# Kernel tuning notes

Hardware: AMD Instinct MI355X
Metric: run time of the kernel (lower is better)

## Reference

```python
import jax, jax.numpy as jnp
import numpy as np

B, T, D = 1, 2048, 1024
H = 16
HD = D // H
K = 4
FF = 4 * D
LAYERS = 24
EPS = 1.1920929e-07  # torch.finfo(float32).eps, RMSNorm default


def setup_inputs() -> dict:
    key = jax.random.key(0)
    ks = jax.random.split(key, 16)
    s = 0.02
    return {
        "x": jax.random.normal(ks[0], (B, T, D), jnp.float32),
        "gamma": jax.random.uniform(ks[1], (D,), jnp.float32),
        "beta": jax.random.normal(ks[2], (D,), jnp.float32) * 0.1,
        "iter_scale": jax.random.uniform(ks[3], (1,), jnp.float32),
        "qkv_bases": jax.random.normal(ks[4], (K, 3 * D, D), jnp.float32) * s,
        "o_bases": jax.random.normal(ks[5], (K, D, D), jnp.float32) * s,
        "gate_bases": jax.random.normal(ks[6], (K, FF, D), jnp.float32) * s,
        "up_bases": jax.random.normal(ks[7], (K, FF, D), jnp.float32) * s,
        "down_bases": jax.random.normal(ks[8], (K, D, FF), jnp.float32) * s,
        "alpha_qkv": jax.random.normal(ks[9], (LAYERS, K), jnp.float32) * 0.1 + jnp.eye(LAYERS, K)[:, :K] * 0.0 + jnp.concatenate([jnp.ones((LAYERS, 1)), jnp.zeros((LAYERS, K - 1))], axis=1),
        "alpha_o": jnp.concatenate([jnp.ones((LAYERS, 1)), jnp.zeros((LAYERS, K - 1))], axis=1) + jax.random.normal(ks[10], (LAYERS, K)) * 0.1,
        "alpha_gate": jnp.concatenate([jnp.ones((LAYERS, 1)), jnp.zeros((LAYERS, K - 1))], axis=1) + jax.random.normal(ks[11], (LAYERS, K)) * 0.1,
        "alpha_up": jnp.concatenate([jnp.ones((LAYERS, 1)), jnp.zeros((LAYERS, K - 1))], axis=1) + jax.random.normal(ks[12], (LAYERS, K)) * 0.1,
        "alpha_down": jnp.concatenate([jnp.ones((LAYERS, 1)), jnp.zeros((LAYERS, K - 1))], axis=1) + jax.random.normal(ks[13], (LAYERS, K)) * 0.1,
        "norm1_w": jnp.ones((D,), jnp.float32),
        "norm2_w": jnp.ones((D,), jnp.float32),
        "layer_idx": 5,
    }


def _rmsnorm(x, w):
    return x * jax.lax.rsqrt(jnp.mean(x * x, axis=-1, keepdims=True) + EPS) * w


def reference(x, gamma, beta, iter_scale, qkv_bases, o_bases, gate_bases, up_bases,
              down_bases, alpha_qkv, alpha_o, alpha_gate, alpha_up, alpha_down,
              norm1_w, norm2_w, layer_idx):
    Bx, Tx, Dx = x.shape
    # --- attention sub-block ---
    h = _rmsnorm(x, norm1_w) * gamma + beta
    W_qkv = jnp.einsum('k,kij->ij', alpha_qkv[layer_idx], qkv_bases)  # [3D, D]
    qkv = jnp.einsum('btd,od->bto', h, W_qkv).reshape(Bx, Tx, 3, H, HD)
    qkv = jnp.transpose(qkv, (2, 0, 3, 1, 4))  # [3, B, H, T, HD]
    q, k, v = qkv[0], qkv[1], qkv[2]
    scores = jnp.einsum('bhqd,bhkd->bhqk', q, k) / jnp.sqrt(jnp.asarray(HD, x.dtype))
    causal = jnp.tril(jnp.ones((Tx, Tx), bool))
    scores = jnp.where(causal, scores, jnp.asarray(-jnp.inf, scores.dtype))
    attn = jax.nn.softmax(scores, axis=-1)
    out = jnp.einsum('bhqk,bhkd->bhqd', attn, v)
    out = jnp.transpose(out, (0, 2, 1, 3)).reshape(Bx, Tx, Dx)
    W_o = jnp.einsum('k,kij->ij', alpha_o[layer_idx], o_bases)
    x_attn = x + jnp.einsum('btd,od->bto', out, W_o)
    # --- SwiGLU FFN sub-block ---
    h2 = _rmsnorm(x_attn, norm2_w) * gamma + beta
    W_g = jnp.einsum('k,kij->ij', alpha_gate[layer_idx], gate_bases)
    W_u = jnp.einsum('k,kij->ij', alpha_up[layer_idx], up_bases)
    W_d = jnp.einsum('k,kij->ij', alpha_down[layer_idx], down_bases)
    gate = jnp.einsum('btd,fd->btf', h2, W_g)
    up = jnp.einsum('btd,fd->btf', h2, W_u)
    ffn_out = jnp.einsum('btf,df->btd', jax.nn.silu(gate) * up, W_d)
    block_out = x_attn + ffn_out
    return x + (block_out - x) * iter_scale
```

## Files before the change

### kernel.cpp

```cpp
#include <hip/hip_runtime.h>
#include <hip/hip_bf16.h>
#include <math.h>

typedef __bf16 bf16;
typedef __bf16 bf16x8 __attribute__((ext_vector_type(8)));
typedef __bf16 bf16x4 __attribute__((ext_vector_type(4)));
typedef float f32x4 __attribute__((ext_vector_type(4)));

#define EPSc 1.1920929e-07f
#define LOG2E 1.44269504f

static __device__ __forceinline__ void glds16(const void* g, void* l) {
  __builtin_amdgcn_global_load_lds((const __attribute__((address_space(1))) void*)g,
                                   (__attribute__((address_space(3))) void*)l, 16, 0, 0);
}

static __device__ __forceinline__ bf16x4 comb4(const float* b0, const float* b1,
                                               const float* b2, const float* b3,
                                               float a0, float a1, float a2, float a3) {
  float4 v0 = *(const float4*)b0, v1 = *(const float4*)b1;
  float4 v2 = *(const float4*)b2, v3 = *(const float4*)b3;
  bf16x4 o;
  o[0] = (bf16)(a0*v0.x + a1*v1.x + a2*v2.x + a3*v3.x);
  o[1] = (bf16)(a0*v0.y + a1*v1.y + a2*v2.y + a3*v3.y);
  o[2] = (bf16)(a0*v0.z + a1*v1.z + a2*v2.z + a3*v3.z);
  o[3] = (bf16)(a0*v0.w + a1*v1.w + a2*v2.w + a3*v3.w);
  return o;
}

__global__ __launch_bounds__(256)
void prep1(const float* __restrict__ qkv_b, const float* __restrict__ a_qkv,
           const float* __restrict__ o_b,   const float* __restrict__ a_o,
           const float* __restrict__ x, const float* __restrict__ n1w,
           const float* __restrict__ gamma, const float* __restrict__ beta,
           const int* __restrict__ lidx,
           bf16* __restrict__ Wqkv, bf16* __restrict__ Wo, bf16* __restrict__ hbuf) {
  const int bid = blockIdx.x, tid = threadIdx.x;
  if (bid < 4096) {
    int li = lidx[0];
    const float* base; const float* al; bf16* out; size_t flat, n;
    if (bid < 3072) { base = qkv_b; al = a_qkv; out = Wqkv; flat = (size_t)bid << 10; n = (size_t)3072*1024; }
    else            { base = o_b;   al = a_o;   out = Wo;   flat = (size_t)(bid-3072) << 10; n = (size_t)1024*1024; }
    float a0 = al[li*4], a1 = al[li*4+1], a2 = al[li*4+2], a3 = al[li*4+3];
    size_t off = flat + tid*4;
    bf16x4 o = comb4(base+off, base+n+off, base+2*n+off, base+3*n+off, a0, a1, a2, a3);
    *(bf16x4*)&out[off] = o;
  } else {
    int row = bid - 4096, t = tid;
    const float4* xr = (const float4*)(x + (size_t)row*1024);
    float4 v = xr[t];
    float ss = v.x*v.x + v.y*v.y + v.z*v.z + v.w*v.w;
    #pragma unroll
    for (int off = 32; off > 0; off >>= 1) ss += __shfl_down(ss, off, 64);
    __shared__ float red[4];
    if ((t & 63) == 0) red[t >> 6] = ss;
    __syncthreads();
    float tot = red[0] + red[1] + red[2] + red[3];
    float r = rsqrtf(tot * (1.0f/1024.0f) + EPSc);
    float4 wv = ((const float4*)n1w)[t];
    float4 gv = ((const float4*)gamma)[t];
    float4 bv = ((const float4*)beta)[t];
    bf16x4 o;
    o[0] = (bf16)(v.x*r*wv.x*gv.x + bv.x);
    o[1] = (bf16)(v.y*r*wv.y*gv.y + bv.y);
    o[2] = (bf16)(v.z*r*wv.z*gv.z + bv.z);
    o[3] = (bf16)(v.w*r*wv.w*gv.w + bv.w);
    *(bf16x4*)&hbuf[(size_t)row*1024 + t*4] = o;
  }
}

__global__ __launch_bounds__(256) void rmsnorm_k(const float* __restrict__ x,
                                                 const float* __restrict__ w,
                                                 const float* __restrict__ gamma,
                                                 const float* __restrict__ beta,
                                                 bf16* __restrict__ out) {
  int row = blockIdx.x, t = threadIdx.x;
  const float4* xr = (const float4*)(x + (size_t)row*1024);
  float4 v = xr[t];
  float ss = v.x*v.x + v.y*v.y + v.z*v.z + v.w*v.w;
  #pragma unroll
  for (int off = 32; off > 0; off >>= 1) ss += __shfl_down(ss, off, 64);
  __shared__ float red[4];
  if ((t & 63) == 0) red[t >> 6] = ss;
  __syncthreads();
  float tot = red[0] + red[1] + red[2] + red[3];
  float r = rsqrtf(tot * (1.0f/1024.0f) + EPSc);
  float4 wv = ((const float4*)w)[t];
  float4 gv = ((const float4*)gamma)[t];
  float4 bv = ((const float4*)beta)[t];
  bf16x4 o;
  o[0] = (bf16)(v.x*r*wv.x*gv.x + bv.x);
  o[1] = (bf16)(v.y*r*wv.y*gv.y + bv.y);
  o[2] = (bf16)(v.z*r*wv.z*gv.z + bv.z);
  o[3] = (bf16)(v.w*r*wv.w*gv.w + bv.w);
  *(bf16x4*)&out[(size_t)row*1024 + t*4] = o;
}

template<int EP, int NTW>
__global__ __launch_bounds__(256)
void gemm_bt(const bf16* __restrict__ A, const bf16* __restrict__ Bw,
             int M, int N, int K, int lda, int ldb, int gx,
             float* __restrict__ outf, bf16* __restrict__ outb,
             const float* __restrict__ auxf, const float* __restrict__ auxf2,
             const float* __restrict__ iscale) {
  constexpr int BN = NTW * 32;
  __shared__ __align__(16) bf16 As[2][128*64];
  __shared__ __align__(16) bf16 Bs[2][BN*64];
  const int nwg = gridDim.x;
  const int orig = blockIdx.x;
  const int wg = (orig & 7) * (nwg >> 3) + (orig >> 3);
  const int tn0 = (wg % gx) * BN, tm0 = (wg / gx) * 128;
  const int tid = threadIdx.x, wave = tid >> 6, lane = tid & 63;
  const int lr = lane & 15, lg = lane >> 4;
  const int wr = wave >> 1, wc = wave & 1;
  f32x4 acc[4][NTW] = {};
  const int rs = lane >> 3;
  const int sc = (((lane & 7) ^ rs) << 3);
  const int x0 = ((lg ^ (lr & 7)) << 3);
  const int x1 = (((4 + lg) ^ (lr & 7)) << 3);

  const bf16* Abase = A + (size_t)tm0 * lda;
  const bf16* Bbase = Bw + (size_t)tn0 * ldb;

  auto stage = [&](bf16* as, bf16* bs, int k0) {
    #pragma unroll
    for (int j = 0; j < 4; ++j) {
      int chunk = wave*4 + j;
      int r = chunk*8 + rs;
      glds16(Abase + (size_t)r*lda + k0 + sc, as + chunk*512 + lane*8);
    }
    #pragma unroll
    for (int j = 0; j < NTW; ++j) {
      int chunk = wave*NTW + j;
      int r = chunk*8 + rs;
      glds16(Bbase + (size_t)r*ldb + k0 + sc, bs + chunk*512 + lane*8);
    }
  };
  auto comp = [&](const bf16* as, const bf16* bs) {
    #pragma unroll
    for (int kk = 0; kk < 2; ++kk) {
      const int x = kk ? x1 : x0;
      bf16x8 av[4], bv[NTW];
      #pragma unroll
      for (int m = 0; m < 4; ++m) av[m] = *(const bf16x8*)&as[(wr*64 + m*16 + lr)*64 + x];
      #pragma unroll
      for (int n = 0; n < NTW; ++n) bv[n] = *(const bf16x8*)&bs[(wc*NTW*16 + n*16 + lr)*64 + x];
      #pragma unroll
      for (int m = 0; m < 4; ++m)
        #pragma unroll
        for (int n = 0; n < NTW; ++n)
          acc[m][n] = __builtin_amdgcn_mfma_f32_16x16x32_bf16(av[m], bv[n], acc[m][n], 0, 0, 0);
    }
  };

  bf16 *a0 = As[0], *a1 = As[1], *b0 = Bs[0], *b1 = Bs[1];
  stage(a0, b0, 0);
  __syncthreads();
  for (int k0 = 64; k0 < K; k0 += 64) {
    stage(a1, b1, k0);
    comp(a0, b0);
    __syncthreads();
    bf16* t;
    t = a0; a0 = a1; a1 = t;
    t = b0; b0 = b1; b1 = t;
  }
  comp(a0, b0);

  float its = 0.f;
  if constexpr (EP == 4) its = iscale[0];
  #pragma unroll
  for (int m = 0; m < 4; ++m)
    #pragma unroll
    for (int n = 0; n < NTW; ++n)
      #pragma unroll
      for (int i = 0; i < 4; ++i) {
        int row = tm0 + wr*64 + m*16 + lg*4 + i;
        int col = tn0 + wc*NTW*16 + n*16 + lr;
        size_t idx = (size_t)row * N + col;
        float v = acc[m][n][i];
        if constexpr (EP == 0) outb[idx] = (bf16)v;
        else if constexpr (EP == 1) outf[idx] = auxf[idx] + v;
        else if constexpr (EP == 4) {
          float xv = auxf[idx], xa = auxf2[idx];
          outf[idx] = xv + (xa + v - xv) * its;
        }
      }
}

__global__ __launch_bounds__(512, 2)
void gemm_gu256(const bf16* __restrict__ A, const bf16* __restrict__ Bw,
                bf16* __restrict__ outb) {
  __shared__ __align__(16) bf16 L[2][2][2][8192];
  const int orig = blockIdx.x;
  const int wg = (orig & 7) * 32 + (orig >> 3);
  const int tn0 = (wg & 31) * 256, tm0 = (wg >> 5) * 256;
  const int tid = threadIdx.x, wave = tid >> 6, lane = tid & 63;
  const int lr = lane & 15, lg = lane >> 4;
  const int wr = wave >> 2, wn = wave & 3;
  const int rs8 = lane >> 3;
  const int gc8 = (((lane & 7) ^ rs8) << 3);
  const int xk0 = ((lg ^ (lr & 7)) << 3);
  const int xk1 = (((4 + lg) ^ (lr & 7)) << 3);
  f32x4 acc[8][4] = {};

  const bf16* Ab = A + (size_t)tm0 * 1024;
  const bf16* Bb = Bw + (size_t)tn0 * 1024;

  auto stage_half = [&](bf16* dst, const bf16* gbase, int half, int k0) {
    #pragma unroll
    for (int l = 0; l < 2; ++l) {
      int r = half*128 + (wave*2 + l)*8 + rs8;
      glds16(gbase + (size_t)r*1024 + k0 + gc8, dst + (wave*2 + l)*512 + lane*8);
    }
  };

  stage_half(&L[0][0][0][0], Ab, 0, 0);
  stage_half(&L[0][0][1][0], Ab, 1, 0);
  stage_half(&L[0][1][0][0], Bb, 0, 0);
  stage_half(&L[0][1][1][0], Bb, 1, 0);
  stage_half(&L[1][1][0][0], Bb, 0, 64);
  stage_half(&L[1][1][1][0], Bb, 1, 64);
  asm volatile("s_waitcnt vmcnt(4)" ::: "memory");
  __builtin_amdgcn_s_barrier();

  for (int t = 0; t < 16; ++t) {
    const int b = t & 1;
    const bf16* ah = &L[b][0][wr][0];
    const bf16* bh = &L[b][1][wn >> 1][0];
    bf16x8 breg[4][2];
    #pragma unroll
    for (int p = 0; p < 4; ++p) {
      if (p == 0) {
        #pragma unroll
        for (int n = 0; n < 4; ++n) {
          int row = (wn & 1)*64 + n*16 + lr;
          breg[n][0] = *(const bf16x8*)&bh[row*64 + xk0];
          breg[n][1] = *(const bf16x8*)&bh[row*64 + xk1];
        }
      }
      bf16x8 av[2][2];
      #pragma unroll
      for (int mi = 0; mi < 2; ++mi) {
        int row = p*32 + mi*16 + lr;
        av[mi][0] = *(const bf16x8*)&ah[row*64 + xk0];
        av[mi][1] = *(const bf16x8*)&ah[row*64 + xk1];
      }
      if (p == 0 && t < 15) stage_half(&L[b^1][0][0][0], Ab, 0, (t+1)*64);
      if (p == 1 && t < 15) stage_half(&L[b^1][0][1][0], Ab, 1, (t+1)*64);
      if (p == 2 && t < 14) stage_half(&L[b][1][0][0], Bb, 0, (t+2)*64);
      if (p == 3 && t < 14) stage_half(&L[b][1][1][0], Bb, 1, (t+2)*64);
      __builtin_amdgcn_s_barrier();
      __builtin_amdgcn_s_setprio(1);
      #pragma unroll
      for (int mi = 0; mi < 2; ++mi)
        #pragma unroll
        for (int n = 0; n < 4; ++n) {
          acc[p*2+mi][n] = __builtin_amdgcn_mfma_f32_16x16x32_bf16(av[mi][0], breg[n][0], acc[p*2+mi][n], 0, 0, 0);
          acc[p*2+mi][n] = __builtin_amdgcn_mfma_f32_16x16x32_bf16(av[mi][1], breg[n][1], acc[p*2+mi][n], 0, 0, 0);
        }
      __builtin_amdgcn_s_setprio(0);
      if (p == 3) {
        if (t >= 14) asm volatile("s_waitcnt vmcnt(0)" ::: "memory");
        else         asm volatile("s_waitcnt vmcnt(4)" ::: "memory");
      }
      __builtin_amdgcn_s_barrier();
    }
  }

  #pragma unroll
  for (int mf = 0; mf < 8; ++mf)
    #pragma unroll
    for (int j = 0; j < 2; ++j)
      #pragma unroll
      for (int i = 0; i < 4; ++i) {
        int row = tm0 + wr*128 + mf*16 + lg*4 + i;
        int col = (tn0 >> 1) + wn*32 + j*16 + lr;
        float g = acc[mf][2*j][i], u = acc[mf][2*j+1][i];
        float s = g / (1.f + __builtin_amdgcn_exp2f(-g * LOG2E));
        outb[(size_t)row * 4096 + col] = (bf16)(s * u);
      }
}

__global__ __launch_bounds__(256)
void attn_merge(const float* __restrict__ oPart, const float* __restrict__ mPart,
                const float* __restrict__ lPart, bf16* __restrict__ out) {
  const int q = blockIdx.x, tid = threadIdx.x;
  const int h = tid >> 4;
  const size_t HQ = (size_t)16 * 2048;
  float mA = mPart[h*2048 + q],      mB = mPart[HQ + h*2048 + q];
  float lA = lPart[h*2048 + q],      lB = lPart[HQ + h*2048 + q];
  float fm = fmaxf(mA, mB);
  float eA = __builtin_amdgcn_exp2f(mA - fm);
  float eB = __builtin_amdgcn_exp2f(mB - fm);
  float inv = 1.f / (lA*eA + lB*eB);
  const size_t QD = (size_t)2048 * 1024;
  size_t idx = (size_t)q*1024 + tid*4;
  float4 oA = *(const float4*)&oPart[idx];
  float4 oB = *(const float4*)&oPart[QD + idx];
  bf16x4 o;
  o[0] = (bf16)((oA.x*eA + oB.x*eB) * inv);
  o[1] = (bf16)((oA.y*eA + oB.y*eB) * inv);
  o[2] = (bf16)((oA.z*eA + oB.z*eB) * inv);
  o[3] = (bf16)((oA.w*eA + oB.w*eB) * inv);
  *(bf16x4*)&out[idx] = o;
}

__global__ __launch_bounds__(256)
void attn_mega(const bf16* __restrict__ qkv,
               const float* __restrict__ gate_b, const float* __restrict__ up_b,
               const float* __restrict__ down_b,
               const float* __restrict__ a_gate, const float* __restrict__ a_up,
               const float* __restrict__ a_down, const int* __restrict__ lidx,
               bf16* __restrict__ Wgu, bf16* __restrict__ Wd,
               float* __restrict__ oPart, float* __restrict__ mPart,
               float* __restrict__ lPart) {
  __shared__ __align__(16) bf16 Ks[2][64*72];
  __shared__ __align__(16) bf16 Vt[2][64*66];
  __shared__ __align__(16) bf16 Ps[4][2][16*68];
  const int bid = blockIdx.x;
  const int tid = threadIdx.x;

  if (bid < 256) {
    const int cb = bid;
    int li = lidx[0];
    float g0 = a_gate[li*4], g1 = a_gate[li*4+1], g2 = a_gate[li*4+2], g3 = a_gate[li*4+3];
    float u0 = a_up[li*4],   u1 = a_up[li*4+1],   u2 = a_up[li*4+2],   u3 = a_up[li*4+3];
    float d0 = a_down[li*4], d1 = a_down[li*4+1], d2 = a_down[li*4+2], d3 = a_down[li*4+3];
    const size_t PS = (size_t)4096 * 1024;
    for (int it = 0; it < 48; ++it) {
      int chunk = it * 256 + cb;
      if (chunk < 8192) {
        int r = chunk, w = r & 31;
        int f = ((r >> 5) << 4) + (w & 15);
        const float* base = (w < 16) ? gate_b : up_b;
        float a0 = (w < 16) ? g0 : u0, a1 = (w < 16) ? g1 : u1;
        float a2 = (w < 16) ? g2 : u2, a3 = (w < 16) ? g3 : u3;
        size_t src = (size_t)f*1024 + tid*4;
        bf16x4 o = comb4(base+src, base+PS+src, base+2*PS+src, base+3*PS+src, a0, a1, a2, a3);
        *(bf16x4*)&Wgu[((size_t)r << 10) + tid*4] = o;
      } else {
        size_t off = ((size_t)(chunk - 8192) << 10) + tid*4;
        bf16x4 o = comb4(down_b+off, down_b+PS+off, down_b+2*PS+off, down_b+3*PS+off, d0, d1, d2, d3);
        *(bf16x4*)&Wd[off] = o;
      }
    }
    return;
  }

  const int a = bid - 256;
  const int sp = a >> 8;
  const int rem = a & 255;
  const int qb = 15 - (rem >> 4);
  const int h = rem & 15;
  const int wave = tid >> 6, lane = tid & 63;
  const int lr = lane & 15, lg = lane >> 4;
  const int q0 = qb * 128;
  const int qw = q0 + wave * 32;
  const int t0 = sp * (qb + 1), t1 = t0 + (qb + 1);

  bf16x8 qf[2][2];
  #pragma unroll
  for (int qt = 0; qt < 2; ++qt) {
    const bf16* qrow = qkv + (size_t)(qw + qt*16 + lr)*3072 + h*64;
    qf[qt][0] = *(const bf16x8*)(qrow + lg*8);
    qf[qt][1] = *(const bf16x8*)(qrow + 32 + lg*8);
  }
  f32x4 o[2][4] = {};
  float mrow[2], lrow[2];
  mrow[0] = mrow[1] = -__builtin_inff();
  lrow[0] = lrow[1] = 0.f;
  const int xsrc = (lane & 48) | (lg << 2);

  const int r0 = tid >> 3, r1 = r0 + 32;
  const int c0 = (tid & 7) << 3;
  const bf16* kb = qkv + 1024 + h*64 + c0;
  const bf16* vb = qkv + 2048 + h*64 + c0;

  bf16x8 kreg[2], vreg[2];
  auto stage_load = [&](int kv0) {
    kreg[0] = *(const bf16x8*)(kb + (size_t)(kv0 + r0)*3072);
    kreg[1] = *(const bf16x8*)(kb + (size_t)(kv0 + r1)*3072);
    vreg[0] = *(const bf16x8*)(vb + (size_t)(kv0 + r0)*3072);
    vreg[1] = *(const bf16x8*)(vb + (size_t)(kv0 + r1)*3072);
  };
  auto stage_write = [&](int buf) {
    *(bf16x8*)&Ks[buf][r0*72 + c0] = kreg[0];
    *(bf16x8*)&Ks[buf][r1*72 + c0] = kreg[1];
    #pragma unroll
    for (int e = 0; e < 8; ++e) Vt[buf][(c0 + e)*66 + r0] = vreg[0][e];
    #pragma unroll
    for (int e = 0; e < 8; ++e) Vt[buf][(c0 + e)*66 + r1] = vreg[1][e];
  };

  stage_load(t0 * 64);
  stage_write(0);
  __syncthreads();
  int cur = 0;

  const float C = 0.125f * LOG2E;

  for (int t = t0; t < t1; ++t) {
    const int kv0 = t * 64;
    if (t < t1-1) stage_load(kv0 + 64);

    f32x4 s[2][4] = {};
    __builtin_amdgcn_s_setprio(1);
    #pragma unroll
    for (int n = 0; n < 4; ++n) {
      bf16x8 k0f = *(const bf16x8*)&Ks[cur][(n*16 + lr)*72 + lg*8];
      bf16x8 k1f = *(const bf16x8*)&Ks[cur][(n*16 + lr)*72 + 32 + lg*8];
      #pragma unroll
      for (int qt = 0; qt < 2; ++qt) {
        s[qt][n] = __builtin_amdgcn_mfma_f32_16x16x32_bf16(k0f, qf[qt][0], s[qt][n], 0, 0, 0);
        s[qt][n] = __builtin_amdgcn_mfma_f32_16x16x32_bf16(k1f, qf[qt][1], s[qt][n], 0, 0, 0);
      }
    }
    __builtin_amdgcn_s_setprio(0);

    if (kv0 + 63 > qw) {
      #pragma unroll
      for (int qt = 0; qt < 2; ++qt) {
        const int qv = qw + qt*16 + lr;
        #pragma unroll
        for (int n = 0; n < 4; ++n)
          #pragma unroll
          for (int i = 0; i < 4; ++i)
            if (kv0 + n*16 + lg*4 + i > qv) s[qt][n][i] = -__builtin_inff();
      }
    }

    float pmn[2];
    #pragma unroll
    for (int qt = 0; qt < 2; ++qt) {
      f32x4 u0 = s[qt][0], u1 = s[qt][1];
      #pragma unroll
      for (int i = 0; i < 4; ++i) { u0[i] = fmaxf(u0[i], s[qt][2][i]); u1[i] = fmaxf(u1[i], s[qt][3][i]); }
      float a0 = fmaxf(u0[0], u0[1]), a1 = fmaxf(u0[2], u0[3]);
      float b0 = fmaxf(u1[0], u1[1]), b1 = fmaxf(u1[2], u1[3]);
      float mnew = fmaxf(fmaxf(a0, a1), fmaxf(b0, b1));
      mnew = fmaxf(mnew, __shfl_xor(mnew, 16, 64));
      mnew = fmaxf(mnew, __shfl_xor(mnew, 32, 64));
      pmn[qt] = mnew * C;
    }
    bool grow = (pmn[0] > mrow[0] + 8.f) || (pmn[1] > mrow[1] + 8.f);
    if (__any(grow)) {
      #pragma unroll
      for (int qt = 0; qt < 2; ++qt) {
        float mt = fmaxf(mrow[qt], pmn[qt]);
        float fc = __builtin_amdgcn_exp2f(mrow[qt] - mt);
        mrow[qt] = mt;
        lrow[qt] *= fc;
        #pragma unroll
        for (int i = 0; i < 4; ++i) {
          float fci = __shfl(fc, xsrc + i, 64);
          #pragma unroll
          for (int nd = 0; nd < 4; ++nd) o[qt][nd][i] *= fci;
        }
      }
    }
    #pragma unroll
    for (int qt = 0; qt < 2; ++qt) {
      float mref = fmaxf(mrow[qt], -3e38f);
      float rsum = 0.f;
      #pragma unroll
      for (int n = 0; n < 4; ++n) {
        bf16x4 p4;
        #pragma unroll
        for (int i = 0; i < 4; ++i) {
          float e = __builtin_amdgcn_exp2f(__builtin_fmaf(s[qt][n][i], C, -mref));
          rsum += e;
          p4[i] = (bf16)e;
        }
        *(bf16x4*)&Ps[wave][qt][lr*68 + n*16 + lg*4] = p4;
      }
      rsum += __shfl_xor(rsum, 16, 64);
      rsum += __shfl_xor(rsum, 32, 64);
      lrow[qt] += rsum;
    }
    asm volatile("s_waitcnt lgkmcnt(0)" ::: "memory");

    #pragma unroll
    for (int kk = 0; kk < 2; ++kk) {
      bf16x8 pf0 = *(const bf16x8*)&Ps[wave][0][lr*68 + kk*32 + lg*8];
      bf16x8 pf1 = *(const bf16x8*)&Ps[wave][1][lr*68 + kk*32 + lg*8];
      __builtin_amdgcn_s_setprio(1);
      #pragma unroll
      for (int nd = 0; nd < 4; ++nd) {
        bf16x8 vf = *(const bf16x8*)&Vt[cur][(nd*16 + lr)*66 + kk*32 + lg*8];
        o[0][nd] = __builtin_amdgcn_mfma_f32_16x16x32_bf16(pf0, vf, o[0][nd], 0, 0, 0);
        o[1][nd] = __builtin_amdgcn_mfma_f32_16x16x32_bf16(pf1, vf, o[1][nd], 0, 0, 0);
      }
      __builtin_amdgcn_s_setprio(0);
    }
    if (t < t1-1) {
      stage_write(cur ^ 1);
      __syncthreads();
      cur ^= 1;
    }
  }

  float* oP = oPart + (size_t)sp * 2048 * 1024;
  #pragma unroll
  for (int qt = 0; qt < 2; ++qt) {
    #pragma unroll
    for (int i = 0; i < 4; ++i) {
      size_t row = (size_t)(qw + qt*16 + lg*4 + i)*1024 + h*64;
      #pragma unroll
      for (int nd = 0; nd < 4; ++nd)
        oP[row + nd*16 + lr] = o[qt][nd][i];
    }
    if (lane < 16) {
      size_t si = (size_t)sp * 16 * 2048 + (size_t)h * 2048 + qw + qt*16 + lr;
      mPart[si] = mrow[qt];
      lPart[si] = lrow[qt];
    }
  }
}

extern "C" void kernel_launch(void* const* d_in, const int* in_sizes, int n_in,
                              void* d_out, int out_size, void* d_ws, size_t ws_size,
                              hipStream_t stream) {
  const float* x        = (const float*)d_in[0];
  const float* gamma    = (const float*)d_in[1];
  const float* beta     = (const float*)d_in[2];
  const float* iscale   = (const float*)d_in[3];
  const float* qkv_b    = (const float*)d_in[4];
  const float* o_b      = (const float*)d_in[5];
  const float* gate_b   = (const float*)d_in[6];
  const float* up_b     = (const float*)d_in[7];
  const float* down_b   = (const float*)d_in[8];
  const float* a_qkv    = (const float*)d_in[9];
  const float* a_o      = (const float*)d_in[10];
  const float* a_gate   = (const float*)d_in[11];
  const float* a_up     = (const float*)d_in[12];
  const float* a_down   = (const float*)d_in[13];
  const float* n1w      = (const float*)d_in[14];
  const float* n2w      = (const float*)d_in[15];
  const int*   lidx     = (const int*)d_in[16];

  char* p = (char*)d_ws;
  auto alloc = [&](size_t bytes) { char* r = p; p += (bytes + 255) & ~(size_t)255; return r; };
  bf16*  Wqkv = (bf16*)alloc((size_t)3072*1024*2);
  bf16*  Wo   = (bf16*)alloc((size_t)1024*1024*2);
  bf16*  Wgu  = (bf16*)alloc((size_t)8192*1024*2);
  bf16*  Wd   = (bf16*)alloc((size_t)1024*4096*2);
  bf16*  hbuf = (bf16*)alloc((size_t)2048*1024*2);
  bf16*  qkvb = (bf16*)alloc((size_t)2048*3072*2);
  bf16*  attn = (bf16*)alloc((size_t)2048*1024*2);
  float* xat  = (float*)alloc((size_t)2048*1024*4);
  bf16*  h2   = (bf16*)alloc((size_t)2048*1024*2);
  bf16*  act  = (bf16*)alloc((size_t)2048*4096*2);
  float* oPart = (float*)alloc((size_t)2*2048*1024*4);
  float* mPart = (float*)alloc((size_t)2*16*2048*4);
  float* lPart = (float*)alloc((size_t)2*16*2048*4);
  float* out  = (float*)d_out;

  prep1<<<6144, 256, 0, stream>>>(qkv_b, a_qkv, o_b, a_o, x, n1w, gamma, beta, lidx,
                                  Wqkv, Wo, hbuf);
  gemm_bt<0,4><<<24*16, 256, 0, stream>>>(hbuf, Wqkv, 2048, 3072, 1024, 1024, 1024, 24,
                                          nullptr, qkvb, nullptr, nullptr, nullptr);
  attn_mega<<<768, 256, 0, stream>>>(qkvb, gate_b, up_b, down_b,
                                     a_gate, a_up, a_down, lidx, Wgu, Wd,
                                     oPart, mPart, lPart);
  attn_merge<<<2048, 256, 0, stream>>>(oPart, mPart, lPart, attn);
  gemm_bt<1,2><<<16*16, 256, 0, stream>>>(attn, Wo, 2048, 1024, 1024, 1024, 1024, 16,
                                          xat, nullptr, x, nullptr, nullptr);
  rmsnorm_k<<<2048, 256, 0, stream>>>(xat, n2w, gamma, beta, h2);
  gemm_gu256<<<256, 512, 0, stream>>>(h2, Wgu, act);
  gemm_bt<4,2><<<16*16, 256, 0, stream>>>(act, Wd, 2048, 1024, 4096, 4096, 4096, 16,
                                          out, nullptr, x, xat, iscale);
}
```

Measured before the change: 193.7 us.

## Pre-transpose V and stage K/V into LDS via direct global-to-LDS loads

Adds a separate kernel that transposes V into a head-major [h*64+d][T] buffer before attention. The attention kernel then stages K and pre-transposed V tiles with global_load_lds directly into XOR-swizzled, unpadded LDS buffers. This replaces the register round-trip and the scalar per-element transposed LDS writes. The cost is an extra kernel launch, an extra 4 MB write and read of V, and a changed LDS swizzle scheme that must stay consistent with the MFMA fragment reads.

New measurement: 194.6 us. No clear change (+0.5%).

```diff
diff --git a/kernel.cpp b/kernel.cpp
--- a/kernel.cpp
+++ b/kernel.cpp
@@ -96,6 +96,23 @@
   *(bf16x4*)&out[(size_t)row*1024 + t*4] = o;
 }
 
+__global__ __launch_bounds__(256)
+void transp_v(const bf16* __restrict__ qkvb, bf16* __restrict__ vT) {
+  __shared__ bf16 T[64*72];
+  const int h = blockIdx.x & 15, tb = blockIdx.x >> 4;
+  const int tid = threadIdx.x;
+  const int r = tid >> 3, c0 = (tid & 7) << 3;
+  bf16x8 v0 = *(const bf16x8*)(qkvb + (size_t)(tb*64 + r)*3072 + 2048 + h*64 + c0);
+  bf16x8 v1 = *(const bf16x8*)(qkvb + (size_t)(tb*64 + r + 32)*3072 + 2048 + h*64 + c0);
+  #pragma unroll
+  for (int e = 0; e < 8; ++e) { T[(c0+e)*72 + r] = v0[e]; T[(c0+e)*72 + r + 32] = v1[e]; }
+  __syncthreads();
+  bf16x8 o0 = *(const bf16x8*)&T[r*72 + c0];
+  bf16x8 o1 = *(const bf16x8*)&T[(r+32)*72 + c0];
+  *(bf16x8*)(vT + (size_t)(h*64 + r)*2048 + tb*64 + c0) = o0;
+  *(bf16x8*)(vT + (size_t)(h*64 + r + 32)*2048 + tb*64 + c0) = o1;
+}
+
 template<int EP, int NTW>
 __global__ __launch_bounds__(256)
 void gemm_bt(const bf16* __restrict__ A, const bf16* __restrict__ Bw,
@@ -306,7 +323,7 @@
 }
 
 __global__ __launch_bounds__(256)
-void attn_mega(const bf16* __restrict__ qkv,
+void attn_mega(const bf16* __restrict__ qkv, const bf16* __restrict__ vT,
                const float* __restrict__ gate_b, const float* __restrict__ up_b,
                const float* __restrict__ down_b,
                const float* __restrict__ a_gate, const float* __restrict__ a_up,
@@ -314,8 +331,8 @@
                bf16* __restrict__ Wgu, bf16* __restrict__ Wd,
                float* __restrict__ oPart, float* __restrict__ mPart,
                float* __restrict__ lPart) {
-  __shared__ __align__(16) bf16 Ks[2][64*72];
-  __shared__ __align__(16) bf16 Vt[2][64*66];
+  __shared__ __align__(16) bf16 Ks[2][64*64];
+  __shared__ __align__(16) bf16 VT[2][64*64];
   __shared__ __align__(16) bf16 Ps[4][2][16*68];
   const int bid = blockIdx.x;
   const int tid = threadIdx.x;
@@ -371,29 +388,21 @@
   lrow[0] = lrow[1] = 0.f;
   const int xsrc = (lane & 48) | (lg << 2);
 
-  const int r0 = tid >> 3, r1 = r0 + 32;
-  const int c0 = (tid & 7) << 3;
-  const bf16* kb = qkv + 1024 + h*64 + c0;
-  const bf16* vb = qkv + 2048 + h*64 + c0;
-
-  bf16x8 kreg[2], vreg[2];
-  auto stage_load = [&](int kv0) {
-    kreg[0] = *(const bf16x8*)(kb + (size_t)(kv0 + r0)*3072);
-    kreg[1] = *(const bf16x8*)(kb + (size_t)(kv0 + r1)*3072);
-    vreg[0] = *(const bf16x8*)(vb + (size_t)(kv0 + r0)*3072);
-    vreg[1] = *(const bf16x8*)(vb + (size_t)(kv0 + r1)*3072);
+  const int rs = tid >> 3;
+  const int cs8 = ((tid & 7) ^ (rs & 7)) << 3;
+  const bf16* kb = qkv + 1024 + h*64 + cs8;
+  const bf16* vb = vT + (size_t)(h*64)*2048 + cs8;
+  const int xk0 = ((lg ^ (lr & 7)) << 3);
+  const int xk1 = (((4 + lg) ^ (lr & 7)) << 3);
+
+  auto stage = [&](int buf, int kv0) {
+    glds16(kb + (size_t)(kv0 + rs)*3072,      &Ks[buf][tid*8]);
+    glds16(kb + (size_t)(kv0 + rs + 32)*3072, &Ks[buf][2048 + tid*8]);
+    glds16(vb + (size_t)rs*2048 + kv0,        &VT[buf][tid*8]);
+    glds16(vb + (size_t)(rs + 32)*2048 + kv0, &VT[buf][2048 + tid*8]);
   };
-  auto stage_write = [&](int buf) {
-    *(bf16x8*)&Ks[buf][r0*72 + c0] = kreg[0];
-    *(bf16x8*)&Ks[buf][r1*72 + c0] = kreg[1];
-    #pragma unroll
-    for (int e = 0; e < 8; ++e) Vt[buf][(c0 + e)*66 + r0] = vreg[0][e];
-    #pragma unroll
-    for (int e = 0; e < 8; ++e) Vt[buf][(c0 + e)*66 + r1] = vreg[1][e];
-  };
-
-  stage_load(t0 * 64);
-  stage_write(0);
+
+  stage(0, t0 * 64);
   __syncthreads();
   int cur = 0;
 
@@ -401,14 +410,14 @@
 
   for (int t = t0; t < t1; ++t) {
     const int kv0 = t * 64;
-    if (t < t1-1) stage_load(kv0 + 64);
+    if (t < t1-1) stage(cur ^ 1, kv0 + 64);
 
     f32x4 s[2][4] = {};
     __builtin_amdgcn_s_setprio(1);
     #pragma unroll
     for (int n = 0; n < 4; ++n) {
-      bf16x8 k0f = *(const bf16x8*)&Ks[cur][(n*16 + lr)*72 + lg*8];
-      bf16x8 k1f = *(const bf16x8*)&Ks[cur][(n*16 + lr)*72 + 32 + lg*8];
+      bf16x8 k0f = *(const bf16x8*)&Ks[cur][(n*16 + lr)*64 + xk0];
+      bf16x8 k1f = *(const bf16x8*)&Ks[cur][(n*16 + lr)*64 + xk1];
       #pragma unroll
       for (int qt = 0; qt < 2; ++qt) {
         s[qt][n] = __builtin_amdgcn_mfma_f32_16x16x32_bf16(k0f, qf[qt][0], s[qt][n], 0, 0, 0);
@@ -481,19 +490,19 @@
 
     #pragma unroll
     for (int kk = 0; kk < 2; ++kk) {
+      const int xk = kk ? xk1 : xk0;
       bf16x8 pf0 = *(const bf16x8*)&Ps[wave][0][lr*68 + kk*32 + lg*8];
       bf16x8 pf1 = *(const bf16x8*)&Ps[wave][1][lr*68 + kk*32 + lg*8];
       __builtin_amdgcn_s_setprio(1);
       #pragma unroll
       for (int nd = 0; nd < 4; ++nd) {
-        bf16x8 vf = *(const bf16x8*)&Vt[cur][(nd*16 + lr)*66 + kk*32 + lg*8];
+        bf16x8 vf = *(const bf16x8*)&VT[cur][(nd*16 + lr)*64 + xk];
         o[0][nd] = __builtin_amdgcn_mfma_f32_16x16x32_bf16(pf0, vf, o[0][nd], 0, 0, 0);
         o[1][nd] = __builtin_amdgcn_mfma_f32_16x16x32_bf16(pf1, vf, o[1][nd], 0, 0, 0);
       }
       __builtin_amdgcn_s_setprio(0);
     }
     if (t < t1-1) {
-      stage_write(cur ^ 1);
       __syncthreads();
       cur ^= 1;
     }
@@ -546,6 +555,7 @@
   bf16*  Wd   = (bf16*)alloc((size_t)1024*4096*2);
   bf16*  hbuf = (bf16*)alloc((size_t)2048*1024*2);
   bf16*  qkvb = (bf16*)alloc((size_t)2048*3072*2);
+  bf16*  vTb  = (bf16*)alloc((size_t)1024*2048*2);
   bf16*  attn = (bf16*)alloc((size_t)2048*1024*2);
   float* xat  = (float*)alloc((size_t)2048*1024*4);
   bf16*  h2   = (bf16*)alloc((size_t)2048*1024*2);
@@ -559,7 +569,8 @@
                                   Wqkv, Wo, hbuf);
   gemm_bt<0,4><<<24*16, 256, 0, stream>>>(hbuf, Wqkv, 2048, 3072, 1024, 1024, 1024, 24,
                                           nullptr, qkvb, nullptr, nullptr, nullptr);
-  attn_mega<<<768, 256, 0, stream>>>(qkvb, gate_b, up_b, down_b,
+  transp_v<<<512, 256, 0, stream>>>(qkvb, vTb);
+  attn_mega<<<768, 256, 0, stream>>>(qkvb, vTb, gate_b, up_b, down_b,
                                      a_gate, a_up, a_down, lidx, Wgu, Wd,
                                      oPart, mPart, lPart);
   attn_merge<<<2048, 256, 0, stream>>>(oPart, mPart, lPart, attn);
```
